# Performance work log

Measured on AMD Instinct MI355X. Metric: run time of the kernel, lower is better.

The kernel has to match this reference:

```python
import jax, jax.numpy as jnp
import numpy as np

N_NODES = 100000


def sage_conv(x, src, dst, Wl, bl, Wr):
    # PyG SAGEConv (aggr='mean'): out = lin_l(mean_{j in N(i)} x_j) + lin_r(x_i)
    msg = x[src]                                                   # [E, d] gather
    agg = jax.ops.segment_sum(msg, dst, num_segments=N_NODES)      # [N, d]
    cnt = jax.ops.segment_sum(jnp.ones((src.shape[0], 1), x.dtype), dst,
                              num_segments=N_NODES)                # [N, 1]
    mean = agg / jnp.maximum(cnt, 1.0)
    return mean @ Wl + bl + x @ Wr


def setup_inputs() -> dict:
    key = jax.random.key(0)
    ks = jax.random.split(key, 9)
    N, E, D_IN = N_NODES, 3200000, 64
    x = jax.random.normal(ks[0], (N, D_IN), dtype=jnp.float32)
    edge_index = jax.random.randint(ks[1], (2, E), 0, N, dtype=jnp.int64)

    def glorot(k, fan_in, fan_out):
        lim = float(np.sqrt(6.0 / (fan_in + fan_out)))
        return jax.random.uniform(k, (fan_in, fan_out), jnp.float32, -lim, lim)

    return {
        "x": x,
        "edge_index": edge_index,
        "W1l": glorot(ks[2], D_IN, 64), "b1": jnp.zeros((64,), jnp.float32),
        "W1r": glorot(ks[3], D_IN, 64),
        "W2l": glorot(ks[4], 64, 32), "b2": jnp.zeros((32,), jnp.float32),
        "W2r": glorot(ks[5], 64, 32),
        "W3l": glorot(ks[6], 32, 1), "b3": jnp.zeros((1,), jnp.float32),
        "W3r": glorot(ks[7], 32, 1),
    }


def reference(x, edge_index, W1l, b1, W1r, W2l, b2, W2r, W3l, b3, W3r):
    src, dst = edge_index[0], edge_index[1]
    h = jax.nn.relu(sage_conv(x, src, dst, W1l, b1, W1r))   # dropout: eval mode (identity)
    h = jax.nn.relu(sage_conv(h, src, dst, W2l, b2, W2r))
    h = sage_conv(h, src, dst, W3l, b3, W3r)
    return jax.nn.sigmoid(h)                                # [N, 1]
```

## Files before the change

kernel.cpp:

```cpp
#include <hip/hip_runtime.h>
#include <math.h>

#define NN 100000
#define NB 391
#define BT 8192
#define CAP 12288

typedef float vfloat2 __attribute__((ext_vector_type(2)));
typedef short short8 __attribute__((ext_vector_type(8)));
typedef float floatx4 __attribute__((ext_vector_type(4)));

__device__ __forceinline__ unsigned short f2bf(float f) {
    unsigned int u = __float_as_uint(f);
    u += 0x7fffu + ((u >> 16) & 1u);
    return (unsigned short)(u >> 16);
}

__device__ __forceinline__ unsigned char f2fp8(float f) {
    const int p = __builtin_amdgcn_cvt_pk_fp8_f32(f, f, 0, false);
    return (unsigned char)(p & 0xFF);
}
template <bool HI>
__device__ __forceinline__ vfloat2 fp8pk2(unsigned int w) {
    return __builtin_amdgcn_cvt_pk_f32_fp8((int)w, HI);
}

template <int D_IN, int CL, int CR, int NPB, int FUSE_IN>
__global__ void __launch_bounds__(256)
mlp_mfma_kernel(const float* __restrict__ in0,
                const float* __restrict__ in1,
                const float* __restrict__ Wl,
                const float* __restrict__ Wr,
                const float* __restrict__ bias,
                unsigned char* __restrict__ yout,
                float* __restrict__ zout,
                int n_nodes) {
    constexpr int COLS = CL + CR;
    constexpr int CT = COLS / 16;
    constexpr int KT = D_IN / 32;
    constexpr int NT = NPB / 16;
    constexpr int KG = D_IN / 8;
    __shared__ short sA[NT * KT * 64 * 8];
    __shared__ short sB[CT * KT * 64 * 8];
    __shared__ float sBias[CR];
    const int t = threadIdx.x;
    const int node0 = blockIdx.x * NPB;

    for (int i = t; i < NPB * KG; i += 256) {
        const int nl = i / KG, kg = i % KG;
        const int n = node0 + nl;
        float v[8];
        if (n < n_nodes) {
            const float4* p = (const float4*)(in0 + (long long)n * D_IN + kg * 8);
            float4 a0 = p[0], a1 = p[1];
            if (FUSE_IN) {
                const float4* q = (const float4*)(in1 + (long long)n * D_IN + kg * 8);
                const float4 b0 = q[0], b1 = q[1];
                a0.x = fmaxf(a0.x + b0.x, 0.f); a0.y = fmaxf(a0.y + b0.y, 0.f);
                a0.z = fmaxf(a0.z + b0.z, 0.f); a0.w = fmaxf(a0.w + b0.w, 0.f);
                a1.x = fmaxf(a1.x + b1.x, 0.f); a1.y = fmaxf(a1.y + b1.y, 0.f);
                a1.z = fmaxf(a1.z + b1.z, 0.f); a1.w = fmaxf(a1.w + b1.w, 0.f);
            }
            v[0] = a0.x; v[1] = a0.y; v[2] = a0.z; v[3] = a0.w;
            v[4] = a1.x; v[5] = a1.y; v[6] = a1.z; v[7] = a1.w;
        } else {
#pragma unroll
            for (int j = 0; j < 8; ++j) v[j] = 0.f;
        }
        short8 s;
#pragma unroll
        for (int j = 0; j < 8; ++j) s[j] = (short)f2bf(v[j]);
        const int nt = nl >> 4, m = nl & 15, kt = kg >> 2, quad = kg & 3;
        ((short8*)sA)[(nt * KT + kt) * 64 + quad * 16 + m] = s;
    }
    for (int i = t; i < CT * KT * 64; i += 256) {
        const int ct = i / (KT * 64);
        const int rem = i % (KT * 64);
        const int kt = rem / 64, L = rem % 64;
        const int c = ct * 16 + (L & 15);
        const int k0 = kt * 32 + (L >> 4) * 8;
        short8 s;
#pragma unroll
        for (int j = 0; j < 8; ++j) {
            const int k = k0 + j;
            const float w = (c < CL) ? Wl[k * CL + c] : Wr[k * CR + (c - CL)];
            s[j] = (short)f2bf(w);
        }
        ((short8*)sB)[i] = s;
    }
    for (int i = t; i < CR; i += 256) sBias[i] = bias[i];
    __syncthreads();

    const int w = t >> 6, lane = t & 63;
    short8 Bf[CT][KT];
#pragma unroll
    for (int ct = 0; ct < CT; ++ct)
#pragma unroll
        for (int kt = 0; kt < KT; ++kt)
            Bf[ct][kt] = ((short8*)sB)[(ct * KT + kt) * 64 + lane];
    const int col = lane & 15, quad = lane >> 4;
#pragma unroll
    for (int nti = 0; nti < NT / 4; ++nti) {
        const int nt = w * (NT / 4) + nti;
        short8 A[KT];
#pragma unroll
        for (int kt = 0; kt < KT; ++kt)
            A[kt] = ((short8*)sA)[(nt * KT + kt) * 64 + lane];
        const int nodeb = node0 + nt * 16 + quad * 4;
#pragma unroll
        for (int ct = 0; ct < CT; ++ct) {
            floatx4 acc = {0.f, 0.f, 0.f, 0.f};
#pragma unroll
            for (int kt = 0; kt < KT; ++kt)
                acc = __builtin_amdgcn_mfma_f32_16x16x32_bf16(A[kt], Bf[ct][kt], acc, 0, 0, 0);
            const int gc = ct * 16 + col;
#pragma unroll
            for (int r = 0; r < 4; ++r) {
                const int node = nodeb + r;
                if (node < n_nodes) {
                    if (gc < CL) yout[(long long)node * CL + gc] = f2fp8(acc[r]);
                    else zout[(long long)node * CR + (gc - CL)] = acc[r] + sBias[gc - CL];
                }
            }
        }
    }
}

template <int D_IN>
__global__ void __launch_bounds__(256)
mlp3_kernel(const float* __restrict__ mean,
            const float* __restrict__ z,
            const float* __restrict__ W3l,
            const float* __restrict__ W3r,
            const float* __restrict__ b3,
            float* __restrict__ y,
            float* __restrict__ z3, int n_nodes) {
    __shared__ float swl[D_IN], swr[D_IN];
    const int t = threadIdx.x;
    if (t < D_IN) { swl[t] = W3l[t]; swr[t] = W3r[t]; }
    __syncthreads();
    const int n = blockIdx.x * 256 + t;
    if (n >= n_nodes) return;
    const float4* pm = (const float4*)(mean + (long long)n * D_IN);
    const float4* pz = (const float4*)(z + (long long)n * D_IN);
    float accl = 0.f, accr = 0.f;
#pragma unroll
    for (int q = 0; q < D_IN / 4; ++q) {
        const float4 m4 = pm[q];
        const float4 z4 = pz[q];
        const float h0 = fmaxf(m4.x + z4.x, 0.f);
        const float h1 = fmaxf(m4.y + z4.y, 0.f);
        const float h2 = fmaxf(m4.z + z4.z, 0.f);
        const float h3 = fmaxf(m4.w + z4.w, 0.f);
        accl += h0 * swl[4 * q] + h1 * swl[4 * q + 1] + h2 * swl[4 * q + 2] + h3 * swl[4 * q + 3];
        accr += h0 * swr[4 * q] + h1 * swr[4 * q + 1] + h2 * swr[4 * q + 2] + h3 * swr[4 * q + 3];
    }
    y[n] = accl;
    z3[n] = accr + b3[0];
}

__global__ void sigmoid_out_kernel(const float* __restrict__ mean,
                                   const float* __restrict__ z,
                                   float* __restrict__ out, int n) {
    const int i = blockIdx.x * 256 + threadIdx.x;
    if (i < n) out[i] = 1.0f / (1.0f + expf(-(mean[i] + z[i])));
}

__global__ void bucket_hist_kernel(const int* __restrict__ dst,
                                   int* __restrict__ bcnt, int n_edges) {
    __shared__ int lh[NB];
    for (int i = threadIdx.x; i < NB; i += 256) lh[i] = 0;
    __syncthreads();
    const int stride = gridDim.x * 256;
    for (int i = blockIdx.x * 256 + threadIdx.x; i < n_edges; i += stride)
        atomicAdd(&lh[dst[i] >> 8], 1);
    __syncthreads();
    for (int i = threadIdx.x; i < NB; i += 256)
        if (lh[i]) atomicAdd(&bcnt[i], lh[i]);
}

__global__ void __launch_bounds__(512)
bucket_scan_kernel(const int* __restrict__ bcnt, int* __restrict__ boffs,
                   int* __restrict__ bcursor) {
    __shared__ int s[512];
    const int t = threadIdx.x;
    const int v = (t < NB) ? bcnt[t] : 0;
    s[t] = v;
    __syncthreads();
    for (int off = 1; off < 512; off <<= 1) {
        const int tmp = (t >= off) ? s[t - off] : 0;
        __syncthreads();
        s[t] += tmp;
        __syncthreads();
    }
    const int excl = s[t] - v;
    if (t <= NB) boffs[t] = excl;
    if (t < NB) bcursor[t] = excl;
}

__global__ void __launch_bounds__(512)
bin_edges_kernel(const int* __restrict__ src, const int* __restrict__ dst,
                 int* __restrict__ bcursor, unsigned int* __restrict__ binned,
                 int n_edges) {
    __shared__ unsigned int stage[BT];
    __shared__ unsigned short sbkt[BT];
    __shared__ int lhist[512], lscan[512], lstart[512], gbase[512], lcur[512];
    const int t = threadIdx.x;
    const int e0 = blockIdx.x * BT;
    const int count = min(BT, n_edges - e0);
    lhist[t] = 0;
    __syncthreads();
    for (int i = t; i < count; i += 512) atomicAdd(&lhist[dst[e0 + i] >> 8], 1);
    __syncthreads();
    const int v = lhist[t];
    lscan[t] = v;
    __syncthreads();
    for (int off = 1; off < 512; off <<= 1) {
        const int tmp = (t >= off) ? lscan[t - off] : 0;
        __syncthreads();
        lscan[t] += tmp;
        __syncthreads();
    }
    const int excl = lscan[t] - v;
    lstart[t] = excl;
    lcur[t] = excl;
    if (t < NB && v > 0) gbase[t] = atomicAdd(&bcursor[t], v);
    __syncthreads();
    for (int i = t; i < count; i += 512) {
        const int d = dst[e0 + i];
        const int b = d >> 8;
        const int p = atomicAdd(&lcur[b], 1);
        stage[p] = (unsigned int)src[e0 + i] | ((unsigned int)(d & 255) << 17);
        sbkt[p] = (unsigned short)b;
    }
    __syncthreads();
    for (int i = t; i < count; i += 512) {
        const int b = sbkt[i];
        binned[gbase[b] + (i - lstart[b])] = stage[i];
    }
}

__global__ void __launch_bounds__(1024)
csr_sort_kernel(const unsigned int* __restrict__ binned,
                const int* __restrict__ boffs,
                int* __restrict__ ssrc, int* __restrict__ row_ptr,
                float* __restrict__ inv_deg, int n_nodes, int n_edges) {
    __shared__ int stage[CAP];
    __shared__ int hist[256];
    __shared__ int lexcl[256];
    __shared__ int lcur[256];
    const int t = threadIdx.x;
    const int b = blockIdx.x;
    const int s0 = boffs[b], s1 = boffs[b + 1];
    const int count = s1 - s0;
    if (t < 256) hist[t] = 0;
    __syncthreads();
    for (int i = t; i < count; i += 1024)
        atomicAdd(&hist[binned[s0 + i] >> 17], 1);
    __syncthreads();
    if (t < 256) lexcl[t] = hist[t];
    __syncthreads();
    for (int off = 1; off < 256; off <<= 1) {
        int tmp = 0;
        if (t < 256 && t >= off) tmp = lexcl[t - off];
        __syncthreads();
        if (t < 256) lexcl[t] += tmp;
        __syncthreads();
    }
    if (t < 256) {
        const int excl = lexcl[t] - hist[t];
        lcur[t] = excl;
        const int n = (b << 8) + t;
        if (n < n_nodes) {
            row_ptr[n] = s0 + excl;
            inv_deg[n] = 1.0f / (float)max(hist[t], 1);
        }
    }
    if (b == NB - 1 && t == 0) row_ptr[n_nodes] = n_edges;
    __syncthreads();
    for (int i = t; i < count; i += 1024) {
        const unsigned int v = binned[s0 + i];
        const int p = atomicAdd(&lcur[v >> 17], 1);
        if (p < CAP) stage[p] = (int)(v & 0x1FFFFu);
    }
    __syncthreads();
    for (int i = t; i < count; i += 1024) ssrc[s0 + i] = stage[i];
}

template <int D>
__global__ void agg_mean_fp8_kernel(const unsigned int* __restrict__ yb,
                                    const int* __restrict__ row_ptr,
                                    const int* __restrict__ ssrc,
                                    const float* __restrict__ inv_deg,
                                    float* __restrict__ mean, int n_nodes) {
    constexpr int G = D / 16;
    constexpr int NPB = 256 / G;
    const int g = threadIdx.x / G;
    const int lane = threadIdx.x % G;
    const int n = blockIdx.x * NPB + g;
    if (n >= n_nodes) return;
    const int s0 = row_ptr[n], s1 = row_ptr[n + 1];
    const uint4* yv = (const uint4*)yb;
    float acc[16];
#pragma unroll
    for (int i = 0; i < 16; ++i) acc[i] = 0.f;
    int e = s0;
    for (; e + 4 <= s1; e += 4) {
        uint4 v[4];
        v[0] = yv[(long long)ssrc[e] * G + lane];
        v[1] = yv[(long long)ssrc[e + 1] * G + lane];
        v[2] = yv[(long long)ssrc[e + 2] * G + lane];
        v[3] = yv[(long long)ssrc[e + 3] * G + lane];
#pragma unroll
        for (int q = 0; q < 4; ++q) {
            const unsigned int wx = v[q].x, wy = v[q].y, wz = v[q].z, ww = v[q].w;
            vfloat2 p;
            p = fp8pk2<false>(wx); acc[0]  += p.x; acc[1]  += p.y;
            p = fp8pk2<true>(wx);  acc[2]  += p.x; acc[3]  += p.y;
            p = fp8pk2<false>(wy); acc[4]  += p.x; acc[5]  += p.y;
            p = fp8pk2<true>(wy);  acc[6]  += p.x; acc[7]  += p.y;
            p = fp8pk2<false>(wz); acc[8]  += p.x; acc[9]  += p.y;
            p = fp8pk2<true>(wz);  acc[10] += p.x; acc[11] += p.y;
            p = fp8pk2<false>(ww); acc[12] += p.x; acc[13] += p.y;
            p = fp8pk2<true>(ww);  acc[14] += p.x; acc[15] += p.y;
        }
    }
    for (; e < s1; ++e) {
        const uint4 v = yv[(long long)ssrc[e] * G + lane];
        vfloat2 p;
        p = fp8pk2<false>(v.x); acc[0]  += p.x; acc[1]  += p.y;
        p = fp8pk2<true>(v.x);  acc[2]  += p.x; acc[3]  += p.y;
        p = fp8pk2<false>(v.y); acc[4]  += p.x; acc[5]  += p.y;
        p = fp8pk2<true>(v.y);  acc[6]  += p.x; acc[7]  += p.y;
        p = fp8pk2<false>(v.z); acc[8]  += p.x; acc[9]  += p.y;
        p = fp8pk2<true>(v.z);  acc[10] += p.x; acc[11] += p.y;
        p = fp8pk2<false>(v.w); acc[12] += p.x; acc[13] += p.y;
        p = fp8pk2<true>(v.w);  acc[14] += p.x; acc[15] += p.y;
    }
    const float inv = inv_deg[n];
    float4* mv = (float4*)mean;
    const long long base = (long long)n * (D / 4) + lane * 4;
#pragma unroll
    for (int q = 0; q < 4; ++q)
        mv[base + q] = make_float4(acc[4 * q] * inv, acc[4 * q + 1] * inv,
                                   acc[4 * q + 2] * inv, acc[4 * q + 3] * inv);
}

__global__ void agg_mean_d1_kernel(const float* __restrict__ y,
                                   const int* __restrict__ row_ptr,
                                   const int* __restrict__ ssrc,
                                   const float* __restrict__ inv_deg,
                                   float* __restrict__ mean, int n_nodes) {
    const int wave = threadIdx.x >> 6;
    const int lane = threadIdx.x & 63;
    const int n = blockIdx.x * 4 + wave;
    if (n >= n_nodes) return;
    const int s0 = row_ptr[n], s1 = row_ptr[n + 1];
    float acc = 0.f;
    for (int e = s0 + lane; e < s1; e += 64) acc += y[ssrc[e]];
    for (int off = 32; off > 0; off >>= 1) acc += __shfl_down(acc, off, 64);
    if (lane == 0) mean[n] = acc * inv_deg[n];
}

extern "C" void kernel_launch(void* const* d_in, const int* in_sizes, int n_in,
                              void* d_out, int out_size, void* d_ws, size_t ws_size,
                              hipStream_t stream) {
    const float* x = (const float*)d_in[0];
    const int* edge_index = (const int*)d_in[1];
    const float* W1l = (const float*)d_in[2];
    const float* b1  = (const float*)d_in[3];
    const float* W1r = (const float*)d_in[4];
    const float* W2l = (const float*)d_in[5];
    const float* b2  = (const float*)d_in[6];
    const float* W2r = (const float*)d_in[7];
    const float* W3l = (const float*)d_in[8];
    const float* b3  = (const float*)d_in[9];
    const float* W3r = (const float*)d_in[10];
    float* out = (float*)d_out;

    const int E = in_sizes[1] / 2;
    const int* src = edge_index;
    const int* dst = edge_index + E;

    float* bufY    = (float*)d_ws;
    float* meanB   = bufY + 32LL * NN;
    float* z1      = meanB + 64LL * NN;
    float* z2      = z1 + 64LL * NN;
    float* z3      = z2 + 32LL * NN;
    float* inv_deg = z3 + NN;
    int* bcnt      = (int*)(inv_deg + NN);
    int* boffs     = bcnt + NB;
    int* bcursor   = boffs + NB + 1;
    int* row_ptr   = bcursor + NB;
    int* ssrc      = row_ptr + NN + 1;
    unsigned int* binned = (unsigned int*)z1;

    const int ntiles = (E + BT - 1) / BT;

    (void)hipMemsetAsync(bcnt, 0, NB * sizeof(int), stream);
    bucket_hist_kernel<<<512, 256, 0, stream>>>(dst, bcnt, E);
    bucket_scan_kernel<<<1, 512, 0, stream>>>(bcnt, boffs, bcursor);
    bin_edges_kernel<<<ntiles, 512, 0, stream>>>(src, dst, bcursor, binned, E);
    csr_sort_kernel<<<NB, 1024, 0, stream>>>(binned, boffs, ssrc, row_ptr, inv_deg, NN, E);

    mlp_mfma_kernel<64, 64, 64, 128, 0><<<(NN + 127) / 128, 256, 0, stream>>>(
        x, nullptr, W1l, W1r, b1, (unsigned char*)bufY, z1, NN);
    agg_mean_fp8_kernel<64><<<(NN + 63) / 64, 256, 0, stream>>>(
        (const unsigned int*)bufY, row_ptr, ssrc, inv_deg, meanB, NN);

    mlp_mfma_kernel<64, 32, 32, 128, 1><<<(NN + 127) / 128, 256, 0, stream>>>(
        meanB, z1, W2l, W2r, b2, (unsigned char*)bufY, z2, NN);
    agg_mean_fp8_kernel<32><<<(NN + 127) / 128, 256, 0, stream>>>(
        (const unsigned int*)bufY, row_ptr, ssrc, inv_deg, meanB, NN);

    mlp3_kernel<32><<<(NN + 255) / 256, 256, 0, stream>>>(
        meanB, z2, W3l, W3r, b3, bufY, z3, NN);
    agg_mean_d1_kernel<<<(NN + 3) / 4, 256, 0, stream>>>(
        bufY, row_ptr, ssrc, inv_deg, meanB, NN);
    sigmoid_out_kernel<<<(NN + 255) / 256, 256, 0, stream>>>(meanB, z3, out, NN);
}
```

Baseline: 303.0 us.

## Split fp8 feature table into column halves for cache-resident gathers; fuse sigmoid

The MLP kernel now writes the fp8 projected features as two separate column-half tables, and the aggregation kernel processes one half per block. Block indices are interleaved so groups of four blocks cover the same nodes for each half. The intent is to shrink the randomly gathered working set per pass so it fits better in cache, with index loads and mean stores marked nontemporal. The final sigmoid is fused into the degree-1 aggregation kernel, which removes one launch and one round trip through memory. In exchange, the source indices are read twice and each gathered segment is narrower.

```diff
diff --git a/kernel.cpp b/kernel.cpp
--- a/kernel.cpp
+++ b/kernel.cpp
@@ -118,8 +118,14 @@
             for (int r = 0; r < 4; ++r) {
                 const int node = nodeb + r;
                 if (node < n_nodes) {
-                    if (gc < CL) yout[(long long)node * CL + gc] = f2fp8(acc[r]);
-                    else zout[(long long)node * CR + (gc - CL)] = acc[r] + sBias[gc - CL];
+                    if (gc < CL) {
+                        constexpr int CH = CL / 2;
+                        const int h = gc / CH;
+                        yout[(size_t)h * n_nodes * CH +
+                             (long long)node * CH + (gc & (CH - 1))] = f2fp8(acc[r]);
+                    } else {
+                        zout[(long long)node * CR + (gc - CL)] = acc[r] + sBias[gc - CL];
+                    }
                 }
             }
         }
@@ -157,13 +163,6 @@
     }
     y[n] = accl;
     z3[n] = accr + b3[0];
-}
-
-__global__ void sigmoid_out_kernel(const float* __restrict__ mean,
-                                   const float* __restrict__ z,
-                                   float* __restrict__ out, int n) {
-    const int i = blockIdx.x * 256 + threadIdx.x;
-    if (i < n) out[i] = 1.0f / (1.0f + expf(-(mean[i] + z[i])));
 }
 
 __global__ void bucket_hist_kernel(const int* __restrict__ dst,
@@ -288,29 +287,35 @@
 }
 
 template <int D>
-__global__ void agg_mean_fp8_kernel(const unsigned int* __restrict__ yb,
-                                    const int* __restrict__ row_ptr,
-                                    const int* __restrict__ ssrc,
-                                    const float* __restrict__ inv_deg,
-                                    float* __restrict__ mean, int n_nodes) {
-    constexpr int G = D / 16;
+__global__ void __launch_bounds__(256)
+agg_mean_fp8_split_kernel(const unsigned int* __restrict__ yb,
+                          const int* __restrict__ row_ptr,
+                          const int* __restrict__ ssrc,
+                          const float* __restrict__ inv_deg,
+                          float* __restrict__ mean, int n_nodes) {
+    constexpr int CH = D / 2;
+    constexpr int G = CH / 16;
     constexpr int NPB = 256 / G;
+    const int bid = blockIdx.x;
+    const int half = (bid >> 2) & 1;
+    const int lb = (bid >> 3) * 4 + (bid & 3);
     const int g = threadIdx.x / G;
     const int lane = threadIdx.x % G;
-    const int n = blockIdx.x * NPB + g;
+    const int n = lb * NPB + g;
     if (n >= n_nodes) return;
     const int s0 = row_ptr[n], s1 = row_ptr[n + 1];
-    const uint4* yv = (const uint4*)yb;
+    const uint4* yv = (const uint4*)yb + (size_t)half * n_nodes * G;
     float acc[16];
 #pragma unroll
     for (int i = 0; i < 16; ++i) acc[i] = 0.f;
     int e = s0;
     for (; e + 4 <= s1; e += 4) {
+        int sidx[4];
+#pragma unroll
+        for (int q = 0; q < 4; ++q) sidx[q] = __builtin_nontemporal_load(ssrc + e + q);
         uint4 v[4];
-        v[0] = yv[(long long)ssrc[e] * G + lane];
-        v[1] = yv[(long long)ssrc[e + 1] * G + lane];
-        v[2] = yv[(long long)ssrc[e + 2] * G + lane];
-        v[3] = yv[(long long)ssrc[e + 3] * G + lane];
+#pragma unroll
+        for (int q = 0; q < 4; ++q) v[q] = yv[(long long)sidx[q] * G + lane];
 #pragma unroll
         for (int q = 0; q < 4; ++q) {
             const unsigned int wx = v[q].x, wy = v[q].y, wz = v[q].z, ww = v[q].w;
@@ -326,7 +331,8 @@
         }
     }
     for (; e < s1; ++e) {
-        const uint4 v = yv[(long long)ssrc[e] * G + lane];
+        const int si = __builtin_nontemporal_load(ssrc + e);
+        const uint4 v = yv[(long long)si * G + lane];
         vfloat2 p;
         p = fp8pk2<false>(v.x); acc[0]  += p.x; acc[1]  += p.y;
         p = fp8pk2<true>(v.x);  acc[2]  += p.x; acc[3]  += p.y;
@@ -338,28 +344,31 @@
         p = fp8pk2<true>(v.w);  acc[14] += p.x; acc[15] += p.y;
     }
     const float inv = inv_deg[n];
-    float4* mv = (float4*)mean;
-    const long long base = (long long)n * (D / 4) + lane * 4;
-#pragma unroll
-    for (int q = 0; q < 4; ++q)
-        mv[base + q] = make_float4(acc[4 * q] * inv, acc[4 * q + 1] * inv,
-                                   acc[4 * q + 2] * inv, acc[4 * q + 3] * inv);
-}
-
-__global__ void agg_mean_d1_kernel(const float* __restrict__ y,
-                                   const int* __restrict__ row_ptr,
-                                   const int* __restrict__ ssrc,
-                                   const float* __restrict__ inv_deg,
-                                   float* __restrict__ mean, int n_nodes) {
+    floatx4* mv = (floatx4*)mean + (long long)n * (D / 4) + half * (CH / 4) + lane * 4;
+#pragma unroll
+    for (int q = 0; q < 4; ++q) {
+        floatx4 o = {acc[4 * q] * inv, acc[4 * q + 1] * inv,
+                     acc[4 * q + 2] * inv, acc[4 * q + 3] * inv};
+        __builtin_nontemporal_store(o, mv + q);
+    }
+}
+
+__global__ void agg_mean_d1_sig_kernel(const float* __restrict__ y,
+                                       const int* __restrict__ row_ptr,
+                                       const int* __restrict__ ssrc,
+                                       const float* __restrict__ inv_deg,
+                                       const float* __restrict__ z3,
+                                       float* __restrict__ out, int n_nodes) {
     const int wave = threadIdx.x >> 6;
     const int lane = threadIdx.x & 63;
     const int n = blockIdx.x * 4 + wave;
     if (n >= n_nodes) return;
     const int s0 = row_ptr[n], s1 = row_ptr[n + 1];
     float acc = 0.f;
-    for (int e = s0 + lane; e < s1; e += 64) acc += y[ssrc[e]];
+    for (int e = s0 + lane; e < s1; e += 64)
+        acc += y[__builtin_nontemporal_load(ssrc + e)];
     for (int off = 32; off > 0; off >>= 1) acc += __shfl_down(acc, off, 64);
-    if (lane == 0) mean[n] = acc * inv_deg[n];
+    if (lane == 0) out[n] = 1.0f / (1.0f + expf(-(acc * inv_deg[n] + z3[n])));
 }
 
 extern "C" void kernel_launch(void* const* d_in, const int* in_sizes, int n_in,
@@ -405,17 +414,24 @@
 
     mlp_mfma_kernel<64, 64, 64, 128, 0><<<(NN + 127) / 128, 256, 0, stream>>>(
         x, nullptr, W1l, W1r, b1, (unsigned char*)bufY, z1, NN);
-    agg_mean_fp8_kernel<64><<<(NN + 63) / 64, 256, 0, stream>>>(
-        (const unsigned int*)bufY, row_ptr, ssrc, inv_deg, meanB, NN);
+    {
+        const int bph = (NN + 127) / 128;
+        const int grid = 8 * ((bph + 3) / 4);
+        agg_mean_fp8_split_kernel<64><<<grid, 256, 0, stream>>>(
+            (const unsigned int*)bufY, row_ptr, ssrc, inv_deg, meanB, NN);
+    }
 
     mlp_mfma_kernel<64, 32, 32, 128, 1><<<(NN + 127) / 128, 256, 0, stream>>>(
         meanB, z1, W2l, W2r, b2, (unsigned char*)bufY, z2, NN);
-    agg_mean_fp8_kernel<32><<<(NN + 127) / 128, 256, 0, stream>>>(
-        (const unsigned int*)bufY, row_ptr, ssrc, inv_deg, meanB, NN);
+    {
+        const int bph = (NN + 255) / 256;
+        const int grid = 8 * ((bph + 3) / 4);
+        agg_mean_fp8_split_kernel<32><<<grid, 256, 0, stream>>>(
+            (const unsigned int*)bufY, row_ptr, ssrc, inv_deg, meanB, NN);
+    }
 
     mlp3_kernel<32><<<(NN + 255) / 256, 256, 0, stream>>>(
         meanB, z2, W3l, W3r, b3, bufY, z3, NN);
-    agg_mean_d1_kernel<<<(NN + 3) / 4, 256, 0, stream>>>(
-        bufY, row_ptr, ssrc, inv_deg, meanB, NN);
-    sigmoid_out_kernel<<<(NN + 255) / 256, 256, 0, stream>>>(meanB, z3, out, NN);
-}
+    agg_mean_d1_sig_kernel<<<(NN + 3) / 4, 256, 0, stream>>>(
+        bufY, row_ptr, ssrc, inv_deg, z3, out, NN);
+}
```

After: 372.6 us. +23.0%, slower.
